# Kernel optimization log

Hardware: AMD Instinct MI355X
Metric: run time of the kernel (lower is better)

The kernel has to match this reference:

```python
import jax, jax.numpy as jnp
import numpy as np

B, T, S, D = 8, 2048, 8, 256


def setup_inputs() -> dict:
    key = jax.random.key(0)
    k1, k2, k3 = jax.random.split(key, 3)
    x = jax.random.normal(k1, (B, T, S, D), dtype=jnp.float32)
    # nn.Linear-style init scale ~ 1/sqrt(fan_in)
    W_in = jax.random.normal(k2, (D, 2 * D), dtype=jnp.float32) / np.sqrt(D)
    b_in = jnp.zeros((2 * D,), dtype=jnp.float32)
    W_out = jax.random.normal(k3, (D, D), dtype=jnp.float32) / np.sqrt(D)
    b_out = jnp.zeros((D,), dtype=jnp.float32)
    return {"x": x, "W_in": W_in, "b_in": b_in, "W_out": W_out, "b_out": b_out}


def reference(x, W_in, b_in, W_out, b_out):
    # in_proj then chunk into gate / candidate (matches torch chunk(2, dim=-1))
    h = jnp.einsum("btsd,de->btse", x, W_in) + b_in  # [B,T,S,2D]
    gate, cand = jnp.split(h, 2, axis=-1)
    alpha = jax.nn.sigmoid(gate)
    cand = jnp.tanh(cand)
    # Diagonal linear recurrence: state_t = a_t * state_{t-1} + b_t
    # with a_t = 1 - alpha_t, b_t = alpha_t * cand_t, state_{-1} = 0.
    a = 1.0 - alpha
    b = alpha * cand

    def combine(c1, c2):
        a1, b1 = c1
        a2, b2 = c2
        return a1 * a2, a2 * b1 + b2

    _, y = jax.lax.associative_scan(combine, (a, b), axis=1)  # [B,T,S,D]
    # dropout is identity in eval mode
    return jnp.einsum("btsd,de->btse", y, W_out) + b_out
```

## Files before the change

kernel.cpp:

```cpp
#include <hip/hip_runtime.h>
#include <hip/hip_bf16.h>
#include <hip/hip_fp16.h>
#include <cstdint>

typedef __attribute__((ext_vector_type(4))) float f32x4;
typedef __attribute__((ext_vector_type(8))) short s16x8;

#define DEVI static __device__ __forceinline__

constexpr int Bc = 8, Tc = 2048, Sc = 8, Dc = 256;
constexpr int Mc = Bc * Tc * Sc;

DEVI unsigned short f2bf(float x) {
  return __bfloat16_as_ushort(__float2bfloat16(x));
}

DEVI f32x4 mfma16(s16x8 a, s16x8 b, f32x4 c) {
  return __builtin_amdgcn_mfma_f32_16x16x32_bf16(a, b, c, 0, 0, 0);
}

DEVI void gld16(const void* g, void* l) {
  __builtin_amdgcn_global_load_lds(
      (const __attribute__((address_space(1))) unsigned int*)g,
      (__attribute__((address_space(3))) unsigned int*)l, 16, 0, 0);
}

__global__ void cvt_x_k(const float* __restrict__ in, unsigned short* __restrict__ out, int n) {
  int i = (blockIdx.x * blockDim.x + threadIdx.x) * 8;
  int stride = gridDim.x * blockDim.x * 8;
  for (; i < n; i += stride) {
    f32x4 a = *(const f32x4*)(in + i);
    f32x4 b = *(const f32x4*)(in + i + 4);
    s16x8 o;
    o[0] = (short)f2bf(a[0]); o[1] = (short)f2bf(a[1]);
    o[2] = (short)f2bf(a[2]); o[3] = (short)f2bf(a[3]);
    o[4] = (short)f2bf(b[0]); o[5] = (short)f2bf(b[1]);
    o[6] = (short)f2bf(b[2]); o[7] = (short)f2bf(b[3]);
    *(s16x8*)(out + i) = o;
  }
}

__global__ void cvtW_k(const float* __restrict__ Win, const float* __restrict__ Wout,
                       unsigned short* __restrict__ wtin, unsigned short* __restrict__ wtout) {
  int tid = blockIdx.x * blockDim.x + threadIdx.x;
  if (tid < 512 * 256) {
    int c = tid >> 8, r = tid & 255;
    wtin[tid] = f2bf(Win[r * 512 + c]);
  } else {
    int t = tid - 512 * 256;
    int c = t >> 8, r = t & 255;
    wtout[t] = f2bf(Wout[r * 256 + c]);
  }
}

__global__ __launch_bounds__(512, 2) void g1scan_k(
    const unsigned short* __restrict__ xb,
    const unsigned short* __restrict__ wt,
    const float* __restrict__ bias,
    unsigned short* __restrict__ yb)
{
  __shared__ unsigned short As[2][8 * 64 * 32];
  __shared__ float segA[2][4][32], segB[2][4][32];

  int bid = blockIdx.x;
  int lb = (bid & 7) * 64 + (bid >> 3);
  int b = lb >> 6, s = (lb >> 3) & 7, dq = lb & 7;
  int tid = threadIdx.x;
  int lane = tid & 63, wave = tid >> 6;
  int rg = wave >> 1, cg = wave & 1;
  int lo = lane & 15, hi = lane >> 4;

  const short* xs = (const short*)xb;
  const short* wsrc = (const short*)wt;
  size_t rowbase = (size_t)b * 16384 + s;

  int cl = cg * 16 + lo;
  int kg = hi * 8;

  s16x8 bGr[8], bCr[8];
  #pragma unroll
  for (int kf = 0; kf < 8; ++kf) {
    bGr[kf] = *(const s16x8*)(wsrc + (size_t)(dq * 32 + cl) * 256 + kf * 32 + kg);
    bCr[kf] = *(const s16x8*)(wsrc + (size_t)(256 + dq * 32 + cl) * 256 + kf * 32 + kg);
  }
  float bg = bias[dq * 32 + cl];
  float bc = bias[256 + dq * 32 + cl];

  const short* pA[4];
  int ldso[4];
  #pragma unroll
  for (int q = 0; q < 4; ++q) {
    int j = q * 512 + tid;
    int kf = j >> 8, rem = j & 255, r = rem >> 2, cc = j & 3;
    pA[q] = xs + (rowbase + (size_t)r * 8) * 256 + kf * 32 + cc * 8;
    ldso[q] = j * 8;
  }
  const size_t ASTRIDE = (size_t)64 * 8 * 256;

  #pragma unroll
  for (int q = 0; q < 4; ++q) gld16(pA[q], (unsigned short*)As[0] + ldso[q]);
  #pragma unroll
  for (int q = 0; q < 4; ++q) gld16(pA[q] + ASTRIDE, (unsigned short*)As[1] + ldso[q]);
  #pragma unroll
  for (int q = 0; q < 4; ++q) pA[q] += 2 * ASTRIDE;

  float stt = 0.f;

  __syncthreads();

  for (int ch = 0; ch < 32; ++ch) {
    int cur = ch & 1;
    const unsigned short* Ab = (const unsigned short*)As[cur];

    f32x4 accG = {}, accC = {};
    #pragma unroll
    for (int kf = 0; kf < 8; ++kf) {
      s16x8 aF = *(const s16x8*)(Ab + kf * 2048 + (rg * 16 + lo) * 32 + kg);
      accG = mfma16(aF, bGr[kf], accG);
      accC = mfma16(aF, bCr[kf], accC);
    }

    float av[4], bv[4];
    #pragma unroll
    for (int r = 0; r < 4; ++r) {
      float g = accG[r] + bg;
      float c = accC[r] + bc;
      float alpha = 1.f / (1.f + __expf(-g));
      float e2 = __expf(2.f * c);
      float th = 1.f - 2.f / (e2 + 1.f);
      av[r] = 1.f - alpha;
      bv[r] = alpha * th;
    }

    float iA = av[0], iB = bv[0];
    #pragma unroll
    for (int r = 1; r < 4; ++r) { iA = iA * av[r]; iB = fmaf(av[r], iB, bv[r]); }

    {
      float tA = __shfl_up(iA, 16), tB = __shfl_up(iB, 16);
      float nA = tA * iA, nB = fmaf(iA, tB, iB);
      if (hi >= 1) { iA = nA; iB = nB; }
      tA = __shfl_up(iA, 32); tB = __shfl_up(iB, 32);
      nA = tA * iA; nB = fmaf(iA, tB, iB);
      if (hi >= 2) { iA = nA; iB = nB; }
    }
    float eA = __shfl_up(iA, 16), eB = __shfl_up(iB, 16);
    if (hi == 0) { eA = 1.f; eB = 0.f; }
    if (hi == 3) { segA[cur][rg][cl] = iA; segB[cur][rg][cl] = iB; }

    __syncthreads();

    if (ch + 2 < 32) {
      #pragma unroll
      for (int q = 0; q < 4; ++q) gld16(pA[q], (unsigned short*)As[cur] + ldso[q]);
      #pragma unroll
      for (int q = 0; q < 4; ++q) pA[q] += ASTRIDE;
    }

    float run = stt, s_w = stt;
    #pragma unroll
    for (int r2 = 0; r2 < 4; ++r2) {
      if (r2 == rg) s_w = run;
      run = fmaf(segA[cur][r2][cl], run, segB[cur][r2][cl]);
    }
    stt = run;

    float sv = fmaf(eA, s_w, eB);
    size_t ybase = (rowbase + (size_t)(ch * 64 + rg * 16 + hi * 4) * 8) * 256 + dq * 32 + cl;
    #pragma unroll
    for (int u = 0; u < 4; ++u) {
      sv = fmaf(av[u], sv, bv[u]);
      yb[ybase + (size_t)u * 8 * 256] = f2bf(sv);
    }
  }
}

__global__ __launch_bounds__(256, 2) void gemm2_k(
    const unsigned short* __restrict__ yb,
    const unsigned short* __restrict__ wt,
    const float* __restrict__ bias,
    float* __restrict__ out)
{
  __shared__ unsigned short As[2][2][128 * 32];
  __shared__ unsigned short Bs[2][2][128 * 32];

  int bid = blockIdx.x;
  int swz = (bid & 7) * 256 + (bid >> 3);
  int mtile = swz >> 1, ctile = swz & 1;
  int tid = threadIdx.x;
  int lane = tid & 63, wave = tid >> 6;
  int wr = wave >> 1, wc = wave & 1;

  const short* ys = (const short*)yb;
  const short* wsrc = (const short*)wt;

  auto STAGE = [&](int buf, int k0) {
    unsigned short* Ad = &As[buf][0][0];
    unsigned short* Bd = &Bs[buf][0][0];
    #pragma unroll
    for (int q = 0; q < 4; ++q) {
      int j = q * 256 + tid;
      int p = j >> 9, r = (j >> 2) & 127, cc = j & 3;
      int koff = k0 + p * 32 + cc * 8;
      gld16(ys + (size_t)(mtile * 128 + r) * 256 + koff, Ad + (size_t)j * 8);
      gld16(wsrc + (size_t)(ctile * 128 + r) * 256 + koff, Bd + (size_t)j * 8);
    }
  };

  f32x4 acc[4][4] = {};

  STAGE(0, 0);
  __syncthreads();
  #pragma unroll
  for (int kk = 0; kk < 4; ++kk) {
    int cur = kk & 1;
    if (kk < 3) STAGE(cur ^ 1, (kk + 1) * 64);
    int kg = (lane >> 4) * 8;
    #pragma unroll
    for (int ks = 0; ks < 2; ++ks) {
      s16x8 aF[4], bF[4];
      #pragma unroll
      for (int mf = 0; mf < 4; ++mf)
        aF[mf] = *(const s16x8*)&As[cur][ks][(wr * 64 + mf * 16 + (lane & 15)) * 32 + kg];
      #pragma unroll
      for (int nf = 0; nf < 4; ++nf)
        bF[nf] = *(const s16x8*)&Bs[cur][ks][(wc * 64 + nf * 16 + (lane & 15)) * 32 + kg];
      #pragma unroll
      for (int mf = 0; mf < 4; ++mf)
        #pragma unroll
        for (int nf = 0; nf < 4; ++nf)
          acc[mf][nf] = mfma16(aF[mf], bF[nf], acc[mf][nf]);
    }
    if (kk < 3) __syncthreads();
  }

  int orow0 = mtile * 128 + wr * 64 + (lane >> 4) * 4;
  #pragma unroll
  for (int nf = 0; nf < 4; ++nf) {
    int col = ctile * 128 + wc * 64 + nf * 16 + (lane & 15);
    float bo = bias[col];
    #pragma unroll
    for (int mf = 0; mf < 4; ++mf) {
      #pragma unroll
      for (int r = 0; r < 4; ++r) {
        int row = orow0 + mf * 16 + r;
        out[(size_t)row * 256 + col] = acc[mf][nf][r] + bo;
      }
    }
  }
}

extern "C" void kernel_launch(void* const* d_in, const int* in_sizes, int n_in,
                              void* d_out, int out_size, void* d_ws, size_t ws_size,
                              hipStream_t stream)
{
  const float* x    = (const float*)d_in[0];
  const float* Win  = (const float*)d_in[1];
  const float* bin  = (const float*)d_in[2];
  const float* Wout = (const float*)d_in[3];
  const float* bout = (const float*)d_in[4];
  float* out = (float*)d_out;
  char* ws = (char*)d_ws;

  unsigned short* wtin  = (unsigned short*)(ws);
  unsigned short* wtout = (unsigned short*)(ws + 262144);
  unsigned short* yb    = (unsigned short*)(ws + 393216);
  unsigned short* xb    = (unsigned short*)(ws + 393216 + (size_t)Mc * 256 * 2);

  cvt_x_k<<<1024, 256, 0, stream>>>(x, xb, Mc * 256);
  cvtW_k<<<768, 256, 0, stream>>>(Win, Wout, wtin, wtout);
  g1scan_k<<<512, 512, 0, stream>>>(xb, wtin, bin, yb);
  gemm2_k<<<2048, 256, 0, stream>>>(yb, wtout, bout, out);
}
```

Before: 172.5 us.

## Shrink LDS tiles in scan and GEMM kernels to raise occupancy

```diff
diff --git a/kernel.cpp b/kernel.cpp
--- a/kernel.cpp
+++ b/kernel.cpp
@@ -53,110 +53,113 @@
   }
 }
 
-__global__ __launch_bounds__(512, 2) void g1scan_k(
+__global__ __launch_bounds__(256, 8) void g1scan_k(
     const unsigned short* __restrict__ xb,
     const unsigned short* __restrict__ wt,
     const float* __restrict__ bias,
     unsigned short* __restrict__ yb)
 {
-  __shared__ unsigned short As[2][8 * 64 * 32];
-  __shared__ float segA[2][4][32], segB[2][4][32];
+  __shared__ unsigned short As[2][2 * 64 * 32];
+  __shared__ float segA[2][4][16], segB[2][4][16];
 
   int bid = blockIdx.x;
-  int lb = (bid & 7) * 64 + (bid >> 3);
-  int b = lb >> 6, s = (lb >> 3) & 7, dq = lb & 7;
+  int lb = (bid & 7) * 128 + (bid >> 3);
+  int b = lb >> 7, s = (lb >> 4) & 7, dq = lb & 15;
   int tid = threadIdx.x;
-  int lane = tid & 63, wave = tid >> 6;
-  int rg = wave >> 1, cg = wave & 1;
+  int lane = tid & 63, rg = tid >> 6;
   int lo = lane & 15, hi = lane >> 4;
+  int cl = lo;
+  int kg = hi * 8;
 
   const short* xs = (const short*)xb;
   const short* wsrc = (const short*)wt;
   size_t rowbase = (size_t)b * 16384 + s;
 
-  int cl = cg * 16 + lo;
-  int kg = hi * 8;
-
   s16x8 bGr[8], bCr[8];
   #pragma unroll
   for (int kf = 0; kf < 8; ++kf) {
-    bGr[kf] = *(const s16x8*)(wsrc + (size_t)(dq * 32 + cl) * 256 + kf * 32 + kg);
-    bCr[kf] = *(const s16x8*)(wsrc + (size_t)(256 + dq * 32 + cl) * 256 + kf * 32 + kg);
-  }
-  float bg = bias[dq * 32 + cl];
-  float bc = bias[256 + dq * 32 + cl];
-
-  const short* pA[4];
-  int ldso[4];
-  #pragma unroll
-  for (int q = 0; q < 4; ++q) {
-    int j = q * 512 + tid;
-    int kf = j >> 8, rem = j & 255, r = rem >> 2, cc = j & 3;
-    pA[q] = xs + (rowbase + (size_t)r * 8) * 256 + kf * 32 + cc * 8;
+    bGr[kf] = *(const s16x8*)(wsrc + (size_t)(dq * 16 + cl) * 256 + kf * 32 + kg);
+    bCr[kf] = *(const s16x8*)(wsrc + (size_t)(256 + dq * 16 + cl) * 256 + kf * 32 + kg);
+  }
+  float bg = bias[dq * 16 + cl];
+  float bc = bias[256 + dq * 16 + cl];
+
+  const short* pA[2];
+  int ldso[2];
+  #pragma unroll
+  for (int q = 0; q < 2; ++q) {
+    int j = q * 256 + tid;
+    int kfl = j >> 8, rem = j & 255, r = rem >> 2, cc = j & 3;
+    pA[q] = xs + (rowbase + (size_t)r * 8) * 256 + kfl * 32 + cc * 8;
     ldso[q] = j * 8;
   }
   const size_t ASTRIDE = (size_t)64 * 8 * 256;
 
   #pragma unroll
-  for (int q = 0; q < 4; ++q) gld16(pA[q], (unsigned short*)As[0] + ldso[q]);
-  #pragma unroll
-  for (int q = 0; q < 4; ++q) gld16(pA[q] + ASTRIDE, (unsigned short*)As[1] + ldso[q]);
-  #pragma unroll
-  for (int q = 0; q < 4; ++q) pA[q] += 2 * ASTRIDE;
+  for (int q = 0; q < 2; ++q) gld16(pA[q], (unsigned short*)As[0] + ldso[q]);
+  #pragma unroll
+  for (int q = 0; q < 2; ++q) gld16(pA[q] + 64, (unsigned short*)As[1] + ldso[q]);
+  #pragma unroll
+  for (int q = 0; q < 2; ++q) pA[q] += 128;
 
   float stt = 0.f;
 
   __syncthreads();
 
   for (int ch = 0; ch < 32; ++ch) {
+    f32x4 accG = {}, accC = {};
+    float av[4], bv[4], eA, eB;
+
+    #pragma unroll
+    for (int sub = 0; sub < 4; ++sub) {
+      int buf = sub & 1;
+      const unsigned short* Ab = (const unsigned short*)As[buf];
+      #pragma unroll
+      for (int kfl = 0; kfl < 2; ++kfl) {
+        int kf = sub * 2 + kfl;
+        s16x8 aF = *(const s16x8*)(Ab + kfl * 2048 + (rg * 16 + lo) * 32 + kg);
+        accG = mfma16(aF, bGr[kf], accG);
+        accC = mfma16(aF, bCr[kf], accC);
+      }
+
+      if (sub == 3) {
+        #pragma unroll
+        for (int r = 0; r < 4; ++r) {
+          float g = accG[r] + bg;
+          float c = accC[r] + bc;
+          float alpha = 1.f / (1.f + __expf(-g));
+          float e2 = __expf(2.f * c);
+          float th = 1.f - 2.f / (e2 + 1.f);
+          av[r] = 1.f - alpha;
+          bv[r] = alpha * th;
+        }
+        float iA = av[0], iB = bv[0];
+        #pragma unroll
+        for (int r = 1; r < 4; ++r) { iA = iA * av[r]; iB = fmaf(av[r], iB, bv[r]); }
+        {
+          float tA = __shfl_up(iA, 16), tB = __shfl_up(iB, 16);
+          float nA = tA * iA, nB = fmaf(iA, tB, iB);
+          if (hi >= 1) { iA = nA; iB = nB; }
+          tA = __shfl_up(iA, 32); tB = __shfl_up(iB, 32);
+          nA = tA * iA; nB = fmaf(iA, tB, iB);
+          if (hi >= 2) { iA = nA; iB = nB; }
+        }
+        eA = __shfl_up(iA, 16); eB = __shfl_up(iB, 16);
+        if (hi == 0) { eA = 1.f; eB = 0.f; }
+        if (hi == 3) { segA[ch & 1][rg][cl] = iA; segB[ch & 1][rg][cl] = iB; }
+      }
+
+      __syncthreads();
+
+      if (!(ch == 31 && sub >= 2)) {
+        #pragma unroll
+        for (int q = 0; q < 2; ++q) gld16(pA[q], (unsigned short*)As[buf] + ldso[q]);
+        #pragma unroll
+        for (int q = 0; q < 2; ++q) pA[q] += (sub == 1) ? (ASTRIDE - 192) : 64;
+      }
+    }
+
     int cur = ch & 1;
-    const unsigned short* Ab = (const unsigned short*)As[cur];
-
-    f32x4 accG = {}, accC = {};
-    #pragma unroll
-    for (int kf = 0; kf < 8; ++kf) {
-      s16x8 aF = *(const s16x8*)(Ab + kf * 2048 + (rg * 16 + lo) * 32 + kg);
-      accG = mfma16(aF, bGr[kf], accG);
-      accC = mfma16(aF, bCr[kf], accC);
-    }
-
-    float av[4], bv[4];
-    #pragma unroll
-    for (int r = 0; r < 4; ++r) {
-      float g = accG[r] + bg;
-      float c = accC[r] + bc;
-      float alpha = 1.f / (1.f + __expf(-g));
-      float e2 = __expf(2.f * c);
-      float th = 1.f - 2.f / (e2 + 1.f);
-      av[r] = 1.f - alpha;
-      bv[r] = alpha * th;
-    }
-
-    float iA = av[0], iB = bv[0];
-    #pragma unroll
-    for (int r = 1; r < 4; ++r) { iA = iA * av[r]; iB = fmaf(av[r], iB, bv[r]); }
-
-    {
-      float tA = __shfl_up(iA, 16), tB = __shfl_up(iB, 16);
-      float nA = tA * iA, nB = fmaf(iA, tB, iB);
-      if (hi >= 1) { iA = nA; iB = nB; }
-      tA = __shfl_up(iA, 32); tB = __shfl_up(iB, 32);
-      nA = tA * iA; nB = fmaf(iA, tB, iB);
-      if (hi >= 2) { iA = nA; iB = nB; }
-    }
-    float eA = __shfl_up(iA, 16), eB = __shfl_up(iB, 16);
-    if (hi == 0) { eA = 1.f; eB = 0.f; }
-    if (hi == 3) { segA[cur][rg][cl] = iA; segB[cur][rg][cl] = iB; }
-
-    __syncthreads();
-
-    if (ch + 2 < 32) {
-      #pragma unroll
-      for (int q = 0; q < 4; ++q) gld16(pA[q], (unsigned short*)As[cur] + ldso[q]);
-      #pragma unroll
-      for (int q = 0; q < 4; ++q) pA[q] += ASTRIDE;
-    }
-
     float run = stt, s_w = stt;
     #pragma unroll
     for (int r2 = 0; r2 < 4; ++r2) {
@@ -166,7 +169,7 @@
     stt = run;
 
     float sv = fmaf(eA, s_w, eB);
-    size_t ybase = (rowbase + (size_t)(ch * 64 + rg * 16 + hi * 4) * 8) * 256 + dq * 32 + cl;
+    size_t ybase = (rowbase + (size_t)(ch * 64 + rg * 16 + hi * 4) * 8) * 256 + dq * 16 + cl;
     #pragma unroll
     for (int u = 0; u < 4; ++u) {
       sv = fmaf(av[u], sv, bv[u]);
@@ -175,14 +178,14 @@
   }
 }
 
-__global__ __launch_bounds__(256, 2) void gemm2_k(
+__global__ __launch_bounds__(256, 4) void gemm2_k(
     const unsigned short* __restrict__ yb,
     const unsigned short* __restrict__ wt,
     const float* __restrict__ bias,
     float* __restrict__ out)
 {
-  __shared__ unsigned short As[2][2][128 * 32];
-  __shared__ unsigned short Bs[2][2][128 * 32];
+  __shared__ unsigned short As[2][128 * 32];
+  __shared__ unsigned short Bs[2][128 * 32];
 
   int bid = blockIdx.x;
   int swz = (bid & 7) * 256 + (bid >> 3);
@@ -194,17 +197,15 @@
   const short* ys = (const short*)yb;
   const short* wsrc = (const short*)wt;
 
+  int srow = tid >> 2, sch = (tid & 3) * 8;
+  size_t gArow = (size_t)(mtile * 128 + srow) * 256;
+  size_t gBrow = (size_t)(ctile * 128 + srow) * 256;
+
   auto STAGE = [&](int buf, int k0) {
-    unsigned short* Ad = &As[buf][0][0];
-    unsigned short* Bd = &Bs[buf][0][0];
-    #pragma unroll
-    for (int q = 0; q < 4; ++q) {
-      int j = q * 256 + tid;
-      int p = j >> 9, r = (j >> 2) & 127, cc = j & 3;
-      int koff = k0 + p * 32 + cc * 8;
-      gld16(ys + (size_t)(mtile * 128 + r) * 256 + koff, Ad + (size_t)j * 8);
-      gld16(wsrc + (size_t)(ctile * 128 + r) * 256 + koff, Bd + (size_t)j * 8);
-    }
+    gld16(ys + gArow + k0 + sch,                    &As[buf][(size_t)tid * 8]);
+    gld16(ys + gArow + (size_t)64 * 256 + k0 + sch, &As[buf][2048 + (size_t)tid * 8]);
+    gld16(wsrc + gBrow + k0 + sch,                    &Bs[buf][(size_t)tid * 8]);
+    gld16(wsrc + gBrow + (size_t)64 * 256 + k0 + sch, &Bs[buf][2048 + (size_t)tid * 8]);
   };
 
   f32x4 acc[4][4] = {};
@@ -212,26 +213,23 @@
   STAGE(0, 0);
   __syncthreads();
   #pragma unroll
-  for (int kk = 0; kk < 4; ++kk) {
+  for (int kk = 0; kk < 8; ++kk) {
     int cur = kk & 1;
-    if (kk < 3) STAGE(cur ^ 1, (kk + 1) * 64);
+    if (kk < 7) STAGE(cur ^ 1, (kk + 1) * 32);
     int kg = (lane >> 4) * 8;
-    #pragma unroll
-    for (int ks = 0; ks < 2; ++ks) {
-      s16x8 aF[4], bF[4];
-      #pragma unroll
-      for (int mf = 0; mf < 4; ++mf)
-        aF[mf] = *(const s16x8*)&As[cur][ks][(wr * 64 + mf * 16 + (lane & 15)) * 32 + kg];
+    s16x8 aF[4], bF[4];
+    #pragma unroll
+    for (int mf = 0; mf < 4; ++mf)
+      aF[mf] = *(const s16x8*)&As[cur][(wr * 64 + mf * 16 + (lane & 15)) * 32 + kg];
+    #pragma unroll
+    for (int nf = 0; nf < 4; ++nf)
+      bF[nf] = *(const s16x8*)&Bs[cur][(wc * 64 + nf * 16 + (lane & 15)) * 32 + kg];
+    #pragma unroll
+    for (int mf = 0; mf < 4; ++mf)
       #pragma unroll
       for (int nf = 0; nf < 4; ++nf)
-        bF[nf] = *(const s16x8*)&Bs[cur][ks][(wc * 64 + nf * 16 + (lane & 15)) * 32 + kg];
-      #pragma unroll
-      for (int mf = 0; mf < 4; ++mf)
-        #pragma unroll
-        for (int nf = 0; nf < 4; ++nf)
-          acc[mf][nf] = mfma16(aF[mf], bF[nf], acc[mf][nf]);
-    }
-    if (kk < 3) __syncthreads();
+        acc[mf][nf] = mfma16(aF[mf], bF[nf], acc[mf][nf]);
+    __syncthreads();
   }
 
   int orow0 = mtile * 128 + wr * 64 + (lane >> 4) * 4;
@@ -269,6 +267,6 @@
 
   cvt_x_k<<<1024, 256, 0, stream>>>(x, xb, Mc * 256);
   cvtW_k<<<768, 256, 0, stream>>>(Win, Wout, wtin, wtout);
-  g1scan_k<<<512, 512, 0, stream>>>(xb, wtin, bin, yb);
+  g1scan_k<<<1024, 256, 0, stream>>>(xb, wtin, bin, yb);
   gemm2_k<<<2048, 256, 0, stream>>>(yb, wtout, bout, out);
 }
```

After: 332.7 us. +92.8%, slower.
